# Performance work log

Hardware: AMD Instinct MI355X
Metric: run time of the kernel (lower is better)

The kernel has to match this reference:

```python
import jax, jax.numpy as jnp
import numpy as np

B, S, D = 8, 2048, 768
H1 = 512
EMBED_DIM = 768  # scale = sqrt(embed_dim)


def setup_inputs() -> dict:
    key = jax.random.key(0)
    ks = jax.random.split(key, 5)
    q = jax.random.normal(ks[0], (B, S, D), dtype=jnp.float32)
    k = jax.random.normal(ks[1], (B, S, D), dtype=jnp.float32)
    v = jax.random.normal(ks[2], (B, S, D), dtype=jnp.float32)
    W1 = jax.random.normal(ks[3], (D, H1), dtype=jnp.float32) * (1.0 / np.sqrt(D))
    b1 = jnp.zeros((H1,), dtype=jnp.float32)
    W2 = jax.random.normal(ks[4], (H1, 1), dtype=jnp.float32) * (1.0 / np.sqrt(H1))
    b2 = jnp.zeros((1,), dtype=jnp.float32)
    return {"q": q, "k": k, "v": v, "W1": W1, "b1": b1, "W2": W2, "b2": b2}


def reference(q, k, v, W1, b1, W2, b2):
    # MLP gate on v: fc2(tanh(fc1(v))) -> [B, S, 1] -> squeeze -> [B, S]
    g = jnp.tanh(v @ W1 + b1) @ W2 + b2          # [B, S, 1]
    g = g[..., 0][:, None, :]                    # unsqueeze(-2): [B, 1, S]

    # scores scaled by sqrt(seq_len) (q.shape[1]), as in the original
    scores = jnp.einsum("bqd,bkd->bqk", q, k) / jnp.sqrt(
        jnp.asarray(q.shape[1], dtype=q.dtype))  # [B, S, S]

    # first softmax over dim=1 (column-wise over query axis)
    s = jax.nn.softmax(scores, axis=1)           # [B, S, S]

    # blend with column-mean, scale by sqrt(embed_dim)
    s_mean = jnp.mean(s, axis=1, keepdims=True)  # [B, 1, S]
    scale = jnp.sqrt(jnp.asarray(EMBED_DIM, dtype=q.dtype))
    attn_scores = (s * (1.0 - g) + s_mean * g) / scale

    # second softmax over last dim; dropout p=0 is identity
    attn_weights = jax.nn.softmax(attn_scores, axis=-1)

    attn_output = jnp.einsum("bqk,bkd->bqd", attn_weights, v) + q
    return attn_output, attn_weights
```

## Files before the change

### kernel.cpp

```cpp
#include <hip/hip_runtime.h>

#define BATCH 8
#define SEQ   2048
#define DIM   768
#define HID   512

typedef __attribute__((ext_vector_type(8))) short  short8;
typedef __attribute__((ext_vector_type(4))) float  f32x4;

#define BAR()    asm volatile("s_barrier" ::: "memory")
#define WAITL0() asm volatile("s_waitcnt lgkmcnt(0)" ::: "memory")
#define VMC(n)   asm volatile("s_waitcnt vmcnt(" #n ")" ::: "memory")

__device__ __forceinline__ unsigned short f2bf(float f) {
  union { float f; unsigned u; } x; x.f = f;
  return (unsigned short)((x.u + 0x7FFFu + ((x.u >> 16) & 1u)) >> 16);
}
__device__ __forceinline__ float bf2f(unsigned short u) {
  union { unsigned u; float f; } x; x.u = ((unsigned)u) << 16;
  return x.f;
}
__device__ __forceinline__ void gll16(const void* g, void* l) {
  __builtin_amdgcn_global_load_lds(
      (const __attribute__((address_space(1))) void*)g,
      (__attribute__((address_space(3))) void*)l, 16, 0, 0);
}
__device__ __forceinline__ int swz2(int o) { return o ^ (((o >> 8) & 7) << 4); }
__device__ __forceinline__ int swz3(int o) { return o ^ (((o >> 7) & 7) << 4); }

template<int VAR>
__global__ __launch_bounds__(512, 2)
void gemm8(const unsigned short* __restrict__ Ap, const unsigned short* __restrict__ Bp,
           const float* __restrict__ qres, float* __restrict__ Cf,
           const float* __restrict__ bias, const float* __restrict__ W2,
           float* __restrict__ pg, float* __restrict__ pl)
{
  constexpr int K     = (VAR == 2) ? SEQ : DIM;
  constexpr int NT    = K / 64;
  constexpr int NITER = NT / 2;
  constexpr int APB   = (VAR == 0) ? 8192 : (VAR == 1 ? 1536 : 4096);
  constexpr int BPB   = (VAR == 0) ? 1536 : (VAR == 1 ? 8192 : 4096);
  constexpr int GX    = (VAR == 0) ? 2 : (VAR == 1 ? 8 : 3);
  constexpr int GY    = (VAR == 0) ? 64 : 8;
  constexpr int NB    = (VAR == 0) ? 1 : BATCH;
  constexpr int NWG   = GX * GY * NB;

  __shared__ __align__(16) unsigned char LDS[131072];

  int wg = ((blockIdx.x & 7) * (NWG >> 3)) + ((int)blockIdx.x >> 3);
  const int z  = wg / (GX * GY);
  const int r2 = wg % (GX * GY);
  const int by = r2 / GX;
  const int bx = r2 % GX;
  const int brow = by * 256, bcol = bx * 256;

  const int tid  = threadIdx.x;
  const int lane = tid & 63, wid = tid >> 6;
  const int wm   = wid >> 2, wn = wid & 3;
  const int lhi  = lane >> 4, llo = lane & 15;

  const char* Abase;
  const char* Bbase;
  if constexpr (VAR == 0) {
    Abase = (const char*)Ap + (size_t)brow * APB;
    Bbase = (const char*)Bp + (size_t)bcol * BPB;
  } else if constexpr (VAR == 1) {
    Abase = (const char*)(Ap + (size_t)z * SEQ * DIM) + (size_t)brow * APB;
    Bbase = (const char*)(Bp + (size_t)z * SEQ * 4096 + 2048) + (size_t)bcol * BPB;
  } else {
    Abase = (const char*)(Ap + (size_t)z * SEQ * SEQ) + (size_t)brow * APB;
    Bbase = (const char*)(Bp + (size_t)z * (size_t)DIM * SEQ) + (size_t)bcol * BPB;
  }

  int sr[2], sk[2];
  #pragma unroll
  for (int c = 0; c < 2; ++c) {
    int o = wid * 2048 + c * 1024 + lane * 16;
    int a = swz3(o);
    sr[c] = a >> 7; sk[c] = a & 127;
  }
  auto stA = [&](int buf, int hh, int t) {
    #pragma unroll
    for (int c = 0; c < 2; ++c)
      gll16(Abase + (size_t)(hh * 128 + sr[c]) * APB + t * 128 + sk[c],
            LDS + buf * 32768 + hh * 16384 + wid * 2048 + c * 1024);
  };
  auto stB = [&](int buf, int hh, int t) {
    #pragma unroll
    for (int c = 0; c < 2; ++c)
      gll16(Bbase + (size_t)(hh * 128 + sr[c]) * BPB + t * 128 + sk[c],
            LDS + 65536 + buf * 32768 + hh * 16384 + wid * 2048 + c * 1024);
  };

  f32x4 acc[8][4];
  #pragma unroll
  for (int m = 0; m < 8; ++m)
    #pragma unroll
    for (int n = 0; n < 4; ++n)
      acc[m][n] = (f32x4)(0.0f);

  stA(0, 0, 0); stA(0, 1, 0); stB(0, 0, 0); stB(0, 1, 0);
  stB(1, 0, 1); stB(1, 1, 1);
  VMC(4);
  BAR();

  auto ITER = [&](int i, bool last) {
    #pragma unroll
    for (int kk = 0; kk < 2; ++kk) {
      const int buf = kk;
      short8 aR[4][2], b0R[2][2], b1R[2][2];
      #pragma unroll
      for (int ph = 0; ph < 4; ++ph) {
        const int h  = ph >> 1;
        const int nh = (ph == 1 || ph == 2) ? 1 : 0;
        if (ph == 0 || ph == 2) {
          #pragma unroll
          for (int fm = 0; fm < 4; ++fm)
            #pragma unroll
            for (int kh = 0; kh < 2; ++kh) {
              int o = (wm * 128 + h * 64 + fm * 16 + llo) * 128 + kh * 64 + lhi * 16;
              aR[fm][kh] = *(const short8*)(LDS + buf * 32768 + swz3(o));
            }
        }
        if (ph == 0) {
          #pragma unroll
          for (int fn = 0; fn < 2; ++fn)
            #pragma unroll
            for (int kh = 0; kh < 2; ++kh) {
              int o = (wn * 64 + fn * 16 + llo) * 128 + kh * 64 + lhi * 16;
              b0R[fn][kh] = *(const short8*)(LDS + 65536 + buf * 32768 + swz3(o));
            }
        }
        if (ph == 1) {
          #pragma unroll
          for (int fn = 0; fn < 2; ++fn)
            #pragma unroll
            for (int kh = 0; kh < 2; ++kh) {
              int o = (wn * 64 + 32 + fn * 16 + llo) * 128 + kh * 64 + lhi * 16;
              b1R[fn][kh] = *(const short8*)(LDS + 65536 + buf * 32768 + swz3(o));
            }
        }
        const int P = kk * 4 + ph;
        if      (P == 0) stA(1, 0, 2 * i + 1);
        else if (P == 1) stA(1, 1, 2 * i + 1);
        else if (P == 2) { if (!last) stB(0, 0, 2 * i + 2); }
        else if (P == 3) { if (!last) stB(0, 1, 2 * i + 2); }
        else if (P == 4) { if (!last) stA(0, 0, 2 * i + 2); }
        else if (P == 5) { if (!last) stA(0, 1, 2 * i + 2); }
        else if (P == 6) { if (!last) stB(1, 0, 2 * i + 3); }
        else if (P == 7) { if (!last) stB(1, 1, 2 * i + 3); }
        if (P == 3) { if (last) { VMC(0); } else { VMC(4); } }
        if (P == 7) { if (!last) { VMC(4); } }
        BAR();
        WAITL0();
        __builtin_amdgcn_sched_barrier(0);
        __builtin_amdgcn_s_setprio(1);
        #pragma unroll
        for (int kh = 0; kh < 2; ++kh)
          #pragma unroll
          for (int fm = 0; fm < 4; ++fm)
            #pragma unroll
            for (int fn = 0; fn < 2; ++fn)
              acc[h * 4 + fm][nh * 2 + fn] = __builtin_amdgcn_mfma_f32_16x16x32_bf16(
                  aR[fm][kh], nh ? b1R[fn][kh] : b0R[fn][kh],
                  acc[h * 4 + fm][nh * 2 + fn], 0, 0, 0);
        __builtin_amdgcn_s_setprio(0);
        BAR();
      }
    }
  };

  for (int i = 0; i < NITER - 1; ++i) ITER(i, false);
  ITER(NITER - 1, true);

  if constexpr (VAR == 0) {
    float* gredF = (float*)LDS;
    float b1v[4], w2v[4];
    #pragma unroll
    for (int FN = 0; FN < 4; ++FN) {
      int colg = bcol + wn * 64 + FN * 16 + llo;
      b1v[FN] = bias[colg]; w2v[FN] = W2[colg];
    }
    #pragma unroll
    for (int FM = 0; FM < 8; ++FM)
      #pragma unroll
      for (int r = 0; r < 4; ++r) {
        float part = 0.f;
        #pragma unroll
        for (int FN = 0; FN < 4; ++FN)
          part += tanhf(acc[FM][FN][r] + b1v[FN]) * w2v[FN];
        part += __shfl_xor(part, 1);
        part += __shfl_xor(part, 2);
        part += __shfl_xor(part, 4);
        part += __shfl_xor(part, 8);
        if (llo == 0) gredF[(wm * 128 + FM * 16 + lhi * 4 + r) * 4 + wn] = part;
      }
    __syncthreads();
    if (tid < 256)
      pg[(size_t)bx * 16384 + brow + tid] =
          gredF[tid * 4 + 0] + gredF[tid * 4 + 1] + gredF[tid * 4 + 2] + gredF[tid * 4 + 3];
  }
  if constexpr (VAR == 1) {
    const float rs = 0.02209708691207961f;
    unsigned short* C16 = reinterpret_cast<unsigned short*>(Cf);
    float cs[4] = {0.f, 0.f, 0.f, 0.f};
    #pragma unroll
    for (int FM = 0; FM < 8; ++FM)
      #pragma unroll
      for (int r = 0; r < 4; ++r) {
        size_t R = (size_t)z * SEQ + (brow + wm * 128 + FM * 16 + lhi * 4 + r);
        #pragma unroll
        for (int FN = 0; FN < 4; ++FN) {
          int col = bcol + wn * 64 + FN * 16 + llo;
          unsigned short us = f2bf(acc[FM][FN][r] * rs);
          C16[R * 4096 + col] = us;
          cs[FN] += __expf(bf2f(us));
        }
      }
    float* cp = (float*)LDS;
    #pragma unroll
    for (int FN = 0; FN < 4; ++FN) {
      cs[FN] += __shfl_xor(cs[FN], 16);
      cs[FN] += __shfl_xor(cs[FN], 32);
      if (lhi == 0) cp[wm * 256 + wn * 64 + FN * 16 + llo] = cs[FN];
    }
    __syncthreads();
    if (tid < 256)
      pl[(size_t)by * 16384 + z * 2048 + bcol + tid] = cp[tid] + cp[256 + tid];
  }
  if constexpr (VAR == 2) {
    float* C = Cf + (size_t)z * SEQ * DIM;
    const float* Q = qres + (size_t)z * SEQ * DIM;
    #pragma unroll
    for (int FM = 0; FM < 8; ++FM)
      #pragma unroll
      for (int r = 0; r < 4; ++r) {
        int rowg = brow + wm * 128 + FM * 16 + lhi * 4 + r;
        #pragma unroll
        for (int FN = 0; FN < 4; ++FN) {
          int colg = bcol + wn * 64 + FN * 16 + llo;
          C[(size_t)rowg * DIM + colg] = acc[FM][FN][r] + Q[(size_t)rowg * DIM + colg];
        }
      }
  }
}

__global__ __launch_bounds__(256)
void gemm_slow(const float* __restrict__ Wf, const float* __restrict__ Vf,
               const float* __restrict__ qres, float* __restrict__ Cf)
{
  __shared__ __align__(16) unsigned short AsL[128 * 64];
  __shared__ __align__(16) unsigned short BsL[128 * 32];

  const int tid  = threadIdx.x;
  const int z    = blockIdx.z;
  const int brow = blockIdx.y * 128;
  const int bcol = blockIdx.x * 128;
  const int lane = tid & 63;
  const int wid  = tid >> 6;
  const int wr   = (wid >> 1) * 64;
  const int wc   = (wid & 1) * 64;
  const int lhi  = lane >> 4;
  const int llo  = lane & 15;

  const float* AsrcF = Wf + (size_t)z * SEQ * SEQ + (size_t)brow * SEQ;
  const float* BsrcF = Vf + (size_t)z * SEQ * DIM;

  f32x4 acc[4][4];
  #pragma unroll
  for (int m = 0; m < 4; ++m)
    #pragma unroll
    for (int n = 0; n < 4; ++n)
      acc[m][n] = (f32x4)(0.0f);

  for (int k0 = 0; k0 < SEQ; k0 += 32) {
    #pragma unroll
    for (int i = 0; i < 4; ++i) {
      int ob = wid * 4096 + i * 1024;
      int a  = swz3(ob + lane * 16);
      gll16((const char*)AsrcF + (size_t)(a >> 7) * (SEQ * 4) + (size_t)k0 * 4 + (a & 127),
            (char*)AsL + ob);
    }
    {
      int n4 = (tid & 31) << 2;
      int kb = (tid >> 5) << 2;
      float4 r0 = *(const float4*)(BsrcF + (size_t)(k0 + kb + 0) * DIM + bcol + n4);
      float4 r1 = *(const float4*)(BsrcF + (size_t)(k0 + kb + 1) * DIM + bcol + n4);
      float4 r2 = *(const float4*)(BsrcF + (size_t)(k0 + kb + 2) * DIM + bcol + n4);
      float4 r3 = *(const float4*)(BsrcF + (size_t)(k0 + kb + 3) * DIM + bcol + n4);
      float a0[4] = {r0.x, r0.y, r0.z, r0.w};
      float a1[4] = {r1.x, r1.y, r1.z, r1.w};
      float a2[4] = {r2.x, r2.y, r2.z, r2.w};
      float a3[4] = {r3.x, r3.y, r3.z, r3.w};
      #pragma unroll
      for (int jj = 0; jj < 4; ++jj) {
        unsigned lo = (__float_as_uint(a0[jj]) >> 16) | (__float_as_uint(a1[jj]) & 0xFFFF0000u);
        unsigned hi = (__float_as_uint(a2[jj]) >> 16) | (__float_as_uint(a3[jj]) & 0xFFFF0000u);
        int ol = (n4 + jj) * 64 + kb * 2;
        *(uint2*)((char*)BsL + swz2(ol)) = make_uint2(lo, hi);
      }
    }
    __syncthreads();

    short8 af[4], bfr[4];
    #pragma unroll
    for (int m = 0; m < 4; ++m) {
      int row = wr + m * 16 + llo;
      int a0i = row * 128 + lhi * 32;
      f32x4 x = *(const f32x4*)((const char*)AsL + swz3(a0i));
      f32x4 y = *(const f32x4*)((const char*)AsL + swz3(a0i + 16));
      union { unsigned u[4]; short8 s; } r;
      r.u[0] = (__float_as_uint(x[0]) >> 16) | (__float_as_uint(x[1]) & 0xFFFF0000u);
      r.u[1] = (__float_as_uint(x[2]) >> 16) | (__float_as_uint(x[3]) & 0xFFFF0000u);
      r.u[2] = (__float_as_uint(y[0]) >> 16) | (__float_as_uint(y[1]) & 0xFFFF0000u);
      r.u[3] = (__float_as_uint(y[2]) >> 16) | (__float_as_uint(y[3]) & 0xFFFF0000u);
      af[m] = r.s;
    }
    #pragma unroll
    for (int n = 0; n < 4; ++n) {
      int a = (wc + n * 16 + llo) * 64 + lhi * 16;
      bfr[n] = *(const short8*)((const char*)BsL + swz2(a));
    }
    #pragma unroll
    for (int m = 0; m < 4; ++m)
      #pragma unroll
      for (int n = 0; n < 4; ++n)
        acc[m][n] = __builtin_amdgcn_mfma_f32_16x16x32_bf16(af[m], bfr[n], acc[m][n], 0, 0, 0);
    __syncthreads();
  }

  float* C = Cf + (size_t)z * SEQ * DIM;
  const float* Q = qres + (size_t)z * SEQ * DIM;
  #pragma unroll
  for (int m = 0; m < 4; ++m)
    #pragma unroll
    for (int r = 0; r < 4; ++r) {
      int rowg = brow + wr + m * 16 + lhi * 4 + r;
      #pragma unroll
      for (int n = 0; n < 4; ++n) {
        int colg = bcol + wc + n * 16 + llo;
        C[(size_t)rowg * DIM + colg] = acc[m][n][r] + Q[(size_t)rowg * DIM + colg];
      }
    }
}

__global__ __launch_bounds__(256)
void prepack_fused(const float* __restrict__ q, const float* __restrict__ k,
                   const float* __restrict__ v, unsigned short* __restrict__ qb,
                   unsigned short* __restrict__ wsl, unsigned short* __restrict__ vT,
                   int dovT)
{
  __shared__ unsigned short T[64][66];
  const int z  = blockIdx.z;
  const int r0 = blockIdx.y * 64, c0 = blockIdx.x * 64;
  const size_t mb = (size_t)z * SEQ * DIM;
  const int t16 = threadIdx.x & 15, trw = threadIdx.x >> 4;

  #pragma unroll
  for (int j = 0; j < 4; ++j) {
    int row = j * 16 + trw;
    size_t e = mb + (size_t)(r0 + row) * DIM + c0 + t16 * 4;
    float4 qv = *(const float4*)(q + e);
    float4 kv = *(const float4*)(k + e);
    float4 vv = *(const float4*)(v + e);
    ushort4 qo; qo.x = f2bf(qv.x); qo.y = f2bf(qv.y); qo.z = f2bf(qv.z); qo.w = f2bf(qv.w);
    ushort4 ko; ko.x = f2bf(kv.x); ko.y = f2bf(kv.y); ko.z = f2bf(kv.z); ko.w = f2bf(kv.w);
    ushort4 vo; vo.x = f2bf(vv.x); vo.y = f2bf(vv.y); vo.z = f2bf(vv.z); vo.w = f2bf(vv.w);
    *(ushort4*)(qb + e) = qo;
    size_t so = (size_t)(z * SEQ + r0 + row) * 4096 + 2048 + c0 + t16 * 4;
    *(ushort4*)(wsl + so) = ko;
    *(ushort4*)(wsl + so + DIM) = vo;
    *(unsigned*)&T[row][t16 * 4]     = (unsigned)vo.x | ((unsigned)vo.y << 16);
    *(unsigned*)&T[row][t16 * 4 + 2] = (unsigned)vo.z | ((unsigned)vo.w << 16);
  }
  __syncthreads();
  if (dovT) {
    const int tc = threadIdx.x & 63, tr2 = threadIdx.x >> 6;
    unsigned short* vTm = vT + (size_t)z * DIM * SEQ;
    #pragma unroll
    for (int j = 0; j < 16; ++j) {
      int orow = j * 4 + tr2;
      vTm[(size_t)(c0 + orow) * SEQ + r0 + tc] = T[tc][orow];
    }
  }
}

__global__ __launch_bounds__(256)
void transpose_f32_bf16(const float* __restrict__ src, unsigned short* __restrict__ dst,
                        int R, int C)
{
  __shared__ unsigned short T[64][65];
  int r0 = blockIdx.y * 64, c0 = blockIdx.x * 64;
  int tr = threadIdx.x >> 6, tc = threadIdx.x & 63;
  #pragma unroll
  for (int j = 0; j < 16; ++j) {
    int row = j * 4 + tr;
    T[row][tc] = f2bf(src[(size_t)(r0 + row) * C + c0 + tc]);
  }
  __syncthreads();
  #pragma unroll
  for (int j = 0; j < 16; ++j) {
    int row = j * 4 + tr;
    dst[(size_t)(c0 + row) * R + r0 + tc] = T[tc][row];
  }
}

__global__ void finalize(const float* __restrict__ pl, const float* __restrict__ pg,
                         const float* __restrict__ b2, float* __restrict__ lcol,
                         float* __restrict__ g)
{
  int i = blockIdx.x * 256 + threadIdx.x;
  float l = 0.f;
  #pragma unroll
  for (int ch = 0; ch < 8; ++ch) l += pl[ch * 16384 + i];
  lcol[i] = l;
  g[i] = b2[0] + pg[i] + pg[16384 + i];
}

template<bool FAST>
__global__ __launch_bounds__(256)
void rowpass(float* __restrict__ w, const float* __restrict__ lcol,
             const float* __restrict__ gg, unsigned short* __restrict__ wb)
{
  const size_t row = blockIdx.x;
  const int b = (int)(row >> 11);
  const unsigned short* p = (const unsigned short*)w + row * 4096;
  float* wrow = w + row * 2048;
  const int c0 = threadIdx.x * 8;
  const float* lc = lcol + (b << 11);
  const float* gb = gg + (b << 11);

  unsigned short xs[8];
  *(ushort4*)&xs[0] = *(const ushort4*)(p + c0);
  *(ushort4*)&xs[4] = *(const ushort4*)(p + c0 + 4);
  float ls[8], gs[8];
  *(float4*)&ls[0] = *(const float4*)(lc + c0);
  *(float4*)&ls[4] = *(const float4*)(lc + c0 + 4);
  *(float4*)&gs[0] = *(const float4*)(gb + c0);
  *(float4*)&gs[4] = *(const float4*)(gb + c0 + 4);

  float e[8];
  float psum = 0.f;
  #pragma unroll
  for (int j = 0; j < 8; ++j) {
    float s = __expf(bf2f(xs[j])) / ls[j];
    float t = (s * (1.f - gs[j]) + gs[j] * (1.f / 2048.f)) * 0.03608439182435161f;
    float ev = __expf(t);
    e[j] = ev;
    psum += ev;
  }
  #pragma unroll
  for (int off = 1; off < 64; off <<= 1) psum += __shfl_xor(psum, off);
  __shared__ float red[4];
  if ((threadIdx.x & 63) == 0) red[threadIdx.x >> 6] = psum;
  __syncthreads();
  float inv = 1.f / (red[0] + red[1] + red[2] + red[3]);
  float4 o0, o1;
  o0.x = e[0] * inv; o0.y = e[1] * inv; o0.z = e[2] * inv; o0.w = e[3] * inv;
  o1.x = e[4] * inv; o1.y = e[5] * inv; o1.z = e[6] * inv; o1.w = e[7] * inv;
  *(float4*)(wrow + c0) = o0;
  *(float4*)(wrow + c0 + 4) = o1;
  if constexpr (FAST) {
    ushort4 b0, b1v;
    b0.x = f2bf(o0.x); b0.y = f2bf(o0.y); b0.z = f2bf(o0.z); b0.w = f2bf(o0.w);
    b1v.x = f2bf(o1.x); b1v.y = f2bf(o1.y); b1v.z = f2bf(o1.z); b1v.w = f2bf(o1.w);
    *(ushort4*)(wb + row * 2048 + c0) = b0;
    *(ushort4*)(wb + row * 2048 + c0 + 4) = b1v;
  }
}

extern "C" void kernel_launch(void* const* d_in, const int* in_sizes, int n_in,
                              void* d_out, int out_size, void* d_ws, size_t ws_size,
                              hipStream_t stream)
{
  (void)in_sizes; (void)n_in; (void)out_size;
  const float* q  = (const float*)d_in[0];
  const float* k  = (const float*)d_in[1];
  const float* v  = (const float*)d_in[2];
  const float* W1 = (const float*)d_in[3];
  const float* b1 = (const float*)d_in[4];
  const float* W2 = (const float*)d_in[5];
  const float* b2 = (const float*)d_in[6];

  float* out0 = (float*)d_out;
  float* wbuf = out0 + (size_t)BATCH * SEQ * DIM;
  unsigned short* wsl = (unsigned short*)wbuf;
  unsigned short* qb  = (unsigned short*)out0;

  float* g    = (float*)d_ws;
  float* lcol = g + 16384;
  float* pg   = lcol + 16384;
  float* pl   = pg + 65536;
  unsigned short* W1T = (unsigned short*)(pl + 262144);
  unsigned short* vT  = (unsigned short*)((char*)d_ws + 2228224);
  unsigned short* wb  = vT + (size_t)12582912;
  const bool fast = ws_size >= 94502912ull;

  prepack_fused<<<dim3(12, 32, 8), 256, 0, stream>>>(q, k, v, qb, wsl, vT, fast ? 1 : 0);
  transpose_f32_bf16<<<dim3(8, 12, 1), 256, 0, stream>>>(W1, W1T, 768, 512);

  gemm8<0><<<128, 512, 0, stream>>>(wsl + 2816, W1T, nullptr, nullptr, b1, W2, pg, nullptr);
  gemm8<1><<<512, 512, 0, stream>>>(qb, wsl, nullptr, wbuf, nullptr, nullptr, nullptr, pl);

  finalize<<<64, 256, 0, stream>>>(pl, pg, b2, lcol, g);

  if (fast) {
    rowpass<true><<<16384, 256, 0, stream>>>(wbuf, lcol, g, wb);
    gemm8<2><<<192, 512, 0, stream>>>(wb, vT, q, out0, nullptr, nullptr, nullptr, nullptr);
  } else {
    rowpass<false><<<16384, 256, 0, stream>>>(wbuf, lcol, g, nullptr);
    gemm_slow<<<dim3(6, 16, 8), 256, 0, stream>>>(wbuf, v, q, out0);
  }
}
```

Before: 260.9 us.

## Split gate and PV GEMMs into dedicated smaller-tile kernels for more workgroups

Replaces the shared gemm8 variants for the MLP gate GEMM and the final P·V GEMM with specialized kernels. The gate GEMM now uses 256x128 tiles and 256 workgroups (four column partials, so finalize sums four pg slices). The PV GEMM uses 128x192 tiles, giving 512 workgroups instead of 192, with its own LDS double-buffer schedule. The aim is to fill more compute units on the 256-CU device, at the cost of less reuse per tile and more partial-sum traffic.

```diff
diff --git a/kernel.cpp b/kernel.cpp
--- a/kernel.cpp
+++ b/kernel.cpp
@@ -173,33 +173,6 @@
   for (int i = 0; i < NITER - 1; ++i) ITER(i, false);
   ITER(NITER - 1, true);
 
-  if constexpr (VAR == 0) {
-    float* gredF = (float*)LDS;
-    float b1v[4], w2v[4];
-    #pragma unroll
-    for (int FN = 0; FN < 4; ++FN) {
-      int colg = bcol + wn * 64 + FN * 16 + llo;
-      b1v[FN] = bias[colg]; w2v[FN] = W2[colg];
-    }
-    #pragma unroll
-    for (int FM = 0; FM < 8; ++FM)
-      #pragma unroll
-      for (int r = 0; r < 4; ++r) {
-        float part = 0.f;
-        #pragma unroll
-        for (int FN = 0; FN < 4; ++FN)
-          part += tanhf(acc[FM][FN][r] + b1v[FN]) * w2v[FN];
-        part += __shfl_xor(part, 1);
-        part += __shfl_xor(part, 2);
-        part += __shfl_xor(part, 4);
-        part += __shfl_xor(part, 8);
-        if (llo == 0) gredF[(wm * 128 + FM * 16 + lhi * 4 + r) * 4 + wn] = part;
-      }
-    __syncthreads();
-    if (tid < 256)
-      pg[(size_t)bx * 16384 + brow + tid] =
-          gredF[tid * 4 + 0] + gredF[tid * 4 + 1] + gredF[tid * 4 + 2] + gredF[tid * 4 + 3];
-  }
   if constexpr (VAR == 1) {
     const float rs = 0.02209708691207961f;
     unsigned short* C16 = reinterpret_cast<unsigned short*>(Cf);
@@ -228,21 +201,257 @@
     if (tid < 256)
       pl[(size_t)by * 16384 + z * 2048 + bcol + tid] = cp[tid] + cp[256 + tid];
   }
-  if constexpr (VAR == 2) {
-    float* C = Cf + (size_t)z * SEQ * DIM;
-    const float* Q = qres + (size_t)z * SEQ * DIM;
-    #pragma unroll
-    for (int FM = 0; FM < 8; ++FM)
-      #pragma unroll
-      for (int r = 0; r < 4; ++r) {
-        int rowg = brow + wm * 128 + FM * 16 + lhi * 4 + r;
+}
+
+__global__ __launch_bounds__(512, 2)
+void gemm_gate8(const unsigned short* __restrict__ Ap, const unsigned short* __restrict__ Bp,
+                const float* __restrict__ bias, const float* __restrict__ W2,
+                float* __restrict__ pg)
+{
+  constexpr int NITER = 6;
+  __shared__ __align__(16) unsigned char LDS[98304];
+
+  int wg = ((blockIdx.x & 7) * 32) + ((int)blockIdx.x >> 3);
+  const int by = wg >> 2, bx = wg & 3;
+  const int brow = by * 256, bcol = bx * 128;
+
+  const int tid  = threadIdx.x;
+  const int lane = tid & 63, wid = tid >> 6;
+  const int wm   = wid >> 2, wn = wid & 3;
+  const int lhi  = lane >> 4, llo = lane & 15;
+
+  const char* Abase = (const char*)Ap + (size_t)brow * 8192;
+  const char* Bbase = (const char*)Bp + (size_t)bcol * 1536;
+
+  int srA[2], skA[2];
+  #pragma unroll
+  for (int c = 0; c < 2; ++c) {
+    int o = wid * 2048 + c * 1024 + lane * 16;
+    int a = swz3(o);
+    srA[c] = a >> 7; skA[c] = a & 127;
+  }
+  const int o1 = tid * 16;
+  const int a1 = swz3(o1);
+  const int sr1 = a1 >> 7, sk1 = a1 & 127;
+
+  auto stA = [&](int buf, int hh, int t) {
+    #pragma unroll
+    for (int c = 0; c < 2; ++c)
+      gll16(Abase + (size_t)(hh * 128 + srA[c]) * 8192 + t * 128 + skA[c],
+            LDS + buf * 32768 + hh * 16384 + wid * 2048 + c * 1024);
+  };
+  auto stB = [&](int buf, int hh, int t) {
+    gll16(Bbase + (size_t)(hh * 64 + sr1) * 1536 + t * 128 + sk1,
+          LDS + 65536 + buf * 16384 + hh * 8192 + wid * 1024);
+  };
+
+  f32x4 acc[8][2];
+  #pragma unroll
+  for (int m = 0; m < 8; ++m)
+    #pragma unroll
+    for (int n = 0; n < 2; ++n)
+      acc[m][n] = (f32x4)(0.0f);
+
+  stA(0, 0, 0); stA(0, 1, 0); stB(0, 0, 0); stB(0, 1, 0);
+  stB(1, 0, 1); stB(1, 1, 1);
+  VMC(2);
+  BAR();
+
+  auto ITER = [&](int i, bool last) {
+    #pragma unroll
+    for (int kk = 0; kk < 2; ++kk) {
+      const int buf = kk;
+      short8 aR[4][2], b0R[2], b1R[2];
+      #pragma unroll
+      for (int ph = 0; ph < 4; ++ph) {
+        const int h  = ph >> 1;
+        const int nh = (ph == 1 || ph == 2) ? 1 : 0;
+        if (ph == 0 || ph == 2) {
+          #pragma unroll
+          for (int fm = 0; fm < 4; ++fm)
+            #pragma unroll
+            for (int kh = 0; kh < 2; ++kh) {
+              int o = (wm * 128 + h * 64 + fm * 16 + llo) * 128 + kh * 64 + lhi * 16;
+              aR[fm][kh] = *(const short8*)(LDS + buf * 32768 + swz3(o));
+            }
+        }
+        if (ph == 0) {
+          #pragma unroll
+          for (int kh = 0; kh < 2; ++kh) {
+            int o = (wn * 32 + llo) * 128 + kh * 64 + lhi * 16;
+            b0R[kh] = *(const short8*)(LDS + 65536 + buf * 16384 + swz3(o));
+          }
+        }
+        if (ph == 1) {
+          #pragma unroll
+          for (int kh = 0; kh < 2; ++kh) {
+            int o = (wn * 32 + 16 + llo) * 128 + kh * 64 + lhi * 16;
+            b1R[kh] = *(const short8*)(LDS + 65536 + buf * 16384 + swz3(o));
+          }
+        }
+        const int P = kk * 4 + ph;
+        if      (P == 0) stA(1, 0, 2 * i + 1);
+        else if (P == 1) stA(1, 1, 2 * i + 1);
+        else if (P == 2) { if (!last) stB(0, 0, 2 * i + 2); }
+        else if (P == 3) { if (!last) stB(0, 1, 2 * i + 2); }
+        else if (P == 4) { if (!last) stA(0, 0, 2 * i + 2); }
+        else if (P == 5) { if (!last) stA(0, 1, 2 * i + 2); }
+        else if (P == 6) { if (!last) stB(1, 0, 2 * i + 3); }
+        else if (P == 7) { if (!last) stB(1, 1, 2 * i + 3); }
+        if (P == 3) { if (last) { VMC(0); } else { VMC(2); } }
+        if (P == 7) { if (!last) { VMC(2); } }
+        BAR();
+        WAITL0();
+        __builtin_amdgcn_sched_barrier(0);
+        __builtin_amdgcn_s_setprio(1);
         #pragma unroll
-        for (int FN = 0; FN < 4; ++FN) {
-          int colg = bcol + wn * 64 + FN * 16 + llo;
-          C[(size_t)rowg * DIM + colg] = acc[FM][FN][r] + Q[(size_t)rowg * DIM + colg];
+        for (int kh = 0; kh < 2; ++kh)
+          #pragma unroll
+          for (int fm = 0; fm < 4; ++fm)
+            acc[h * 4 + fm][nh] = __builtin_amdgcn_mfma_f32_16x16x32_bf16(
+                aR[fm][kh], nh ? b1R[kh] : b0R[kh], acc[h * 4 + fm][nh], 0, 0, 0);
+        __builtin_amdgcn_s_setprio(0);
+        BAR();
+      }
+    }
+  };
+
+  for (int i = 0; i < NITER - 1; ++i) ITER(i, false);
+  ITER(NITER - 1, true);
+
+  float* gredF = (float*)LDS;
+  float b1v[2], w2v[2];
+  #pragma unroll
+  for (int FN = 0; FN < 2; ++FN) {
+    int colg = bcol + wn * 32 + FN * 16 + llo;
+    b1v[FN] = bias[colg]; w2v[FN] = W2[colg];
+  }
+  #pragma unroll
+  for (int FM = 0; FM < 8; ++FM)
+    #pragma unroll
+    for (int r = 0; r < 4; ++r) {
+      float part = tanhf(acc[FM][0][r] + b1v[0]) * w2v[0]
+                 + tanhf(acc[FM][1][r] + b1v[1]) * w2v[1];
+      part += __shfl_xor(part, 1);
+      part += __shfl_xor(part, 2);
+      part += __shfl_xor(part, 4);
+      part += __shfl_xor(part, 8);
+      if (llo == 0) gredF[(wm * 128 + FM * 16 + lhi * 4 + r) * 4 + wn] = part;
+    }
+  __syncthreads();
+  if (tid < 256)
+    pg[(size_t)bx * 16384 + brow + tid] =
+        gredF[tid * 4 + 0] + gredF[tid * 4 + 1] + gredF[tid * 4 + 2] + gredF[tid * 4 + 3];
+}
+
+__global__ __launch_bounds__(512, 4)
+void gemm_pv(const unsigned short* __restrict__ Ap, const unsigned short* __restrict__ Bp,
+             const float* __restrict__ qres, float* __restrict__ Cf)
+{
+  constexpr int NITER = 16;
+  __shared__ __align__(16) unsigned char LDS[81920];
+
+  int wg = ((blockIdx.x & 7) * 64) + ((int)blockIdx.x >> 3);
+  const int z  = wg >> 6;
+  const int r2 = wg & 63;
+  const int by = r2 >> 2, bx = r2 & 3;
+  const int brow = by * 128, bcol = bx * 192;
+
+  const int tid  = threadIdx.x;
+  const int lane = tid & 63, wid = tid >> 6;
+  const int wm   = wid >> 2, wn = wid & 3;
+  const int lhi  = lane >> 4, llo = lane & 15;
+
+  const char* Abase = (const char*)(Ap + (size_t)z * SEQ * SEQ) + (size_t)brow * 4096;
+  const char* Bbase = (const char*)(Bp + (size_t)z * (size_t)DIM * SEQ) + (size_t)bcol * 4096;
+
+  const int o1 = tid * 16;
+  const int a1 = swz3(o1);
+  const int sr1 = a1 >> 7, sk1 = a1 & 127;
+
+  auto stA = [&](int buf, int u, int t) {
+    gll16(Abase + (size_t)(u * 64 + sr1) * 4096 + t * 128 + sk1,
+          LDS + buf * 16384 + u * 8192 + wid * 1024);
+  };
+  auto stB = [&](int buf, int u, int t) {
+    gll16(Bbase + (size_t)(u * 64 + sr1) * 4096 + t * 128 + sk1,
+          LDS + 32768 + buf * 24576 + u * 8192 + wid * 1024);
+  };
+
+  f32x4 acc[4][3];
+  #pragma unroll
+  for (int m = 0; m < 4; ++m)
+    #pragma unroll
+    for (int n = 0; n < 3; ++n)
+      acc[m][n] = (f32x4)(0.0f);
+
+  stA(0, 0, 0); stA(0, 1, 0);
+  stB(0, 0, 0); stB(0, 1, 0); stB(0, 2, 0);
+  stB(1, 0, 1); stB(1, 1, 1); stB(1, 2, 1);
+  VMC(3);
+  BAR();
+
+  auto ITER = [&](int i, bool last) {
+    short8 aR[2][2], bR[3][2];
+    #pragma unroll
+    for (int ph = 0; ph < 4; ++ph) {
+      const int buf = ph >> 1;
+      const int h   = ph & 1;
+      #pragma unroll
+      for (int fm = 0; fm < 2; ++fm)
+        #pragma unroll
+        for (int kh = 0; kh < 2; ++kh) {
+          int o = (wm * 64 + h * 32 + fm * 16 + llo) * 128 + kh * 64 + lhi * 16;
+          aR[fm][kh] = *(const short8*)(LDS + buf * 16384 + swz3(o));
         }
+      if (h == 0) {
+        #pragma unroll
+        for (int fn = 0; fn < 3; ++fn)
+          #pragma unroll
+          for (int kh = 0; kh < 2; ++kh) {
+            int o = (wn * 48 + fn * 16 + llo) * 128 + kh * 64 + lhi * 16;
+            bR[fn][kh] = *(const short8*)(LDS + 32768 + buf * 24576 + swz3(o));
+          }
       }
-  }
+      if (ph == 0) { stA(1, 0, 2 * i + 1); stA(1, 1, 2 * i + 1); }
+      else if (ph == 1) { if (!last) { stB(0, 0, 2*i+2); stB(0, 1, 2*i+2); stB(0, 2, 2*i+2); } }
+      else if (ph == 2) { if (!last) { stA(0, 0, 2*i+2); stA(0, 1, 2*i+2); } }
+      else              { if (!last) { stB(1, 0, 2*i+3); stB(1, 1, 2*i+3); stB(1, 2, 2*i+3); } }
+      if (ph == 1) { if (last) { VMC(0); } else { VMC(3); } }
+      if (ph == 3) { if (!last) { VMC(3); } }
+      BAR();
+      WAITL0();
+      __builtin_amdgcn_sched_barrier(0);
+      __builtin_amdgcn_s_setprio(1);
+      #pragma unroll
+      for (int kh = 0; kh < 2; ++kh)
+        #pragma unroll
+        for (int fm = 0; fm < 2; ++fm)
+          #pragma unroll
+          for (int fn = 0; fn < 3; ++fn)
+            acc[h * 2 + fm][fn] = __builtin_amdgcn_mfma_f32_16x16x32_bf16(
+                aR[fm][kh], bR[fn][kh], acc[h * 2 + fm][fn], 0, 0, 0);
+      __builtin_amdgcn_s_setprio(0);
+      BAR();
+    }
+  };
+
+  for (int i = 0; i < NITER - 1; ++i) ITER(i, false);
+  ITER(NITER - 1, true);
+
+  float* C = Cf + (size_t)z * SEQ * DIM;
+  const float* Q = qres + (size_t)z * SEQ * DIM;
+  #pragma unroll
+  for (int FM = 0; FM < 4; ++FM)
+    #pragma unroll
+    for (int r = 0; r < 4; ++r) {
+      int rowg = brow + wm * 64 + FM * 16 + lhi * 4 + r;
+      #pragma unroll
+      for (int FN = 0; FN < 3; ++FN) {
+        int colg = bcol + wn * 48 + FN * 16 + llo;
+        C[(size_t)rowg * DIM + colg] = acc[FM][FN][r] + Q[(size_t)rowg * DIM + colg];
+      }
+    }
 }
 
 __global__ __launch_bounds__(256)
@@ -414,7 +623,7 @@
   #pragma unroll
   for (int ch = 0; ch < 8; ++ch) l += pl[ch * 16384 + i];
   lcol[i] = l;
-  g[i] = b2[0] + pg[i] + pg[16384 + i];
+  g[i] = b2[0] + pg[i] + pg[16384 + i] + pg[2 * 16384 + i] + pg[3 * 16384 + i];
 }
 
 template<bool FAST>
@@ -499,14 +708,14 @@
   prepack_fused<<<dim3(12, 32, 8), 256, 0, stream>>>(q, k, v, qb, wsl, vT, fast ? 1 : 0);
   transpose_f32_bf16<<<dim3(8, 12, 1), 256, 0, stream>>>(W1, W1T, 768, 512);
 
-  gemm8<0><<<128, 512, 0, stream>>>(wsl + 2816, W1T, nullptr, nullptr, b1, W2, pg, nullptr);
+  gemm_gate8<<<256, 512, 0, stream>>>(wsl + 2816, W1T, b1, W2, pg);
   gemm8<1><<<512, 512, 0, stream>>>(qb, wsl, nullptr, wbuf, nullptr, nullptr, nullptr, pl);
 
   finalize<<<64, 256, 0, stream>>>(pl, pg, b2, lcol, g);
 
   if (fast) {
     rowpass<true><<<16384, 256, 0, stream>>>(wbuf, lcol, g, wb);
-    gemm8<2><<<192, 512, 0, stream>>>(wb, vT, q, out0, nullptr, nullptr, nullptr, nullptr);
+    gemm_pv<<<512, 512, 0, stream>>>(wb, vT, q, out0);
   } else {
     rowpass<false><<<16384, 256, 0, stream>>>(wbuf, lcol, g, nullptr);
     gemm_slow<<<dim3(6, 16, 8), 256, 0, stream>>>(wbuf, v, q, out0);
```

After: 253.4 us. 1.03x faster.
